# Kernel optimization log

Measured on AMD Instinct MI355X. Metric: run time of the kernel, lower is better.

Reference implementation:

```python
import jax, jax.numpy as jnp
import numpy as np

B, S, E, H, R = 512, 50, 128, 8, 32
D = E // H  # depth per head
USERS, ITEMS, ALLSEQ, NCLASS = 50000, 20000, 20000, 5


def setup_inputs() -> dict:
    key = jax.random.key(0)
    ks = jax.random.split(key, 20)
    n = lambda k, shp, s=0.05: jax.random.normal(k, shp, dtype=jnp.float32) * s
    return {
        "user": jax.random.randint(ks[0], (B,), 0, USERS),
        "item": jax.random.randint(ks[1], (B,), 0, ITEMS),
        "neighbor": jax.random.randint(ks[2], (B, S), 0, USERS),
        "seq": jax.random.randint(ks[3], (B, S), 0, ALLSEQ),
        "user_emb_table": n(ks[4], (USERS, E)),
        "item_emb_table": n(ks[5], (ITEMS, E)),
        "user_item_LCU": n(ks[6], (ALLSEQ, R, E), 0.01),
        "item_user_LCU": n(ks[7], (ALLSEQ, R, E), 0.01),
        "wq": n(ks[8], (E, E)), "bq": jnp.zeros((E,), jnp.float32),
        "wk": n(ks[9], (E, E)), "bk": jnp.zeros((E,), jnp.float32),
        "wv": n(ks[10], (E, E)), "bv": jnp.zeros((E,), jnp.float32),
        "wo": n(ks[11], (E, E)), "bo": jnp.zeros((E,), jnp.float32),
        "fc_w": n(ks[12], (R, NCLASS)), "fc_b": jnp.zeros((NCLASS,), jnp.float32),
    }


def _forward(user, item, neighbor, seq,
             user_emb_table, item_emb_table, user_item_LCU, item_user_LCU,
             wq, bq, wk, bk, wv, bv, wo, bo, fc_w, fc_b):
    user_emb = user_emb_table[user]            # [B,E]
    neighbor_emb = user_emb_table[neighbor]    # [B,S,E]
    item_emb = item_emb_table[item]            # [B,E]
    weight = (neighbor > 0).astype(jnp.float32)  # [B,S] padding mask (1=real)

    # ---- single-query multi-head attention (use_attention=True) ----
    q = (user_emb @ wq + bq).reshape(B, H, D)                       # [B,H,D]
    k = (neighbor_emb @ wk + bk).reshape(B, S, H, D).transpose(0, 2, 1, 3)  # [B,H,S,D]
    v = (neighbor_emb @ wv + bv).reshape(B, S, H, D).transpose(0, 2, 1, 3)  # [B,H,S,D]
    logits = jnp.einsum('bhd,bhsd->bhs', q, k) / jnp.sqrt(jnp.float32(D))
    logits = logits + (1.0 - weight)[:, None, :] * (-1e9)           # mask padding
    attn = jax.nn.softmax(logits, axis=-1)                          # [B,H,S]
    ctx = attn[..., None] * v                                       # [B,H,S,D]
    ctx = ctx.transpose(0, 2, 1, 3).reshape(B, S, E)                # [B,S,E]
    neighbor_emb = ctx @ wo + bo                                    # [B,S,E]

    # ---- region embedding ----
    K_ui = user_item_LCU[seq]   # [B,S,R,E]
    K_iu = item_user_LCU[seq]   # [B,S,R,E]
    neighbor_profile = jnp.einsum('bsre,bse->bsr', K_iu, neighbor_emb)  # [B,S,R]
    item_profile = jnp.einsum('bsre,be->bsr', K_ui, item_emb)          # [B,S,R]
    neighbor_rating = neighbor_profile * item_profile * weight[:, :, None]
    user_rating_vector = jnp.max(neighbor_rating, axis=1)              # [B,R]

    # ---- rating classifier ----
    return jax.nn.softmax(user_rating_vector @ fc_w + fc_b, axis=-1)   # [B,NCLASS]


def reference(user, item, neighbor, seq,
              user_emb_table, item_emb_table, user_item_LCU, item_user_LCU,
              wq, bq, wk, bk, wv, bv, wo, bo, fc_w, fc_b):
    return _forward(user, item, neighbor, seq,
                    user_emb_table, item_emb_table, user_item_LCU, item_user_LCU,
                    wq, bq, wk, bk, wv, bv, wo, bo, fc_w, fc_b)
```

## Files before the change

### kernel.cpp

```cpp
#include <hip/hip_runtime.h>
#include <math.h>

#define BB 512
#define SS 50
#define EE 128
#define HH 8
#define RR 32
#define NC 5
#define NSEQ 20000
#define NBS (BB*SS)
#define LDK 136

typedef __attribute__((ext_vector_type(8))) __bf16 bf16x8;
typedef __attribute__((ext_vector_type(4))) float f32x4;
typedef __attribute__((ext_vector_type(4))) unsigned short us4;

__device__ __forceinline__ unsigned short f2bf(float f) {
    unsigned int u = __float_as_uint(f);
    unsigned int r = (u + 0x7fffu + ((u >> 16) & 1u)) >> 16;
    return (unsigned short)r;
}
__device__ __forceinline__ float dot4(const float4& a, const float4& b) {
    return a.x*b.x + a.y*b.y + a.z*b.z + a.w*b.w;
}
__device__ __forceinline__ float dot4v(const f32x4& a, const float4& b) {
    return a[0]*b.x + a[1]*b.y + a[2]*b.z + a[3]*b.w;
}

__global__ __launch_bounds__(128) void conv_kernel(const float* __restrict__ wv,
                                                   const float* __restrict__ wo,
                                                   unsigned short* __restrict__ wvT,
                                                   unsigned short* __restrict__ woT) {
    const int n = blockIdx.x & 127;
    const float* src = (blockIdx.x >> 7) ? wo : wv;
    unsigned short* dst = (blockIdx.x >> 7) ? woT : wvT;
    const int k = threadIdx.x;
    dst[n*EE + k] = f2bf(src[k*EE + n]);
}

__global__ __launch_bounds__(256) void hist_kernel(const int* __restrict__ seq,
                                                   int* __restrict__ hist) {
    int i = blockIdx.x * 256 + threadIdx.x;
    if (i < NBS) atomicAdd(&hist[seq[i]], 1);
}

__global__ __launch_bounds__(1024) void scan_kernel(int* __restrict__ hist,
                                                    int* __restrict__ hstart) {
    const int t = threadIdx.x;
    const int CH = 20;
    const int base = t * CH;
    int loc[CH];
    int s = 0;
    #pragma unroll
    for (int i = 0; i < CH; ++i) {
        int idx = base + i;
        int v = (idx < NSEQ) ? hist[idx] : 0;
        loc[i] = s; s += v;
    }
    const int lane = t & 63, w = t >> 6;
    int incl = s;
    #pragma unroll
    for (int off = 1; off < 64; off <<= 1) {
        int n = __shfl_up(incl, off);
        if (lane >= off) incl += n;
    }
    __shared__ int wsum[16];
    if (lane == 63) wsum[w] = incl;
    __syncthreads();
    if (t == 0) {
        int acc = 0;
        #pragma unroll
        for (int k = 0; k < 16; ++k) { int v = wsum[k]; wsum[k] = acc; acc += v; }
    }
    __syncthreads();
    const int excl = incl - s + wsum[w];
    #pragma unroll
    for (int i = 0; i < CH; ++i) {
        int idx = base + i;
        if (idx < NSEQ) {
            int e = excl + loc[i];
            hist[idx] = e;
            hstart[idx] = e;
        }
    }
    if (t == 0) hstart[NSEQ] = NBS;
}

__global__ __launch_bounds__(256) void scatter_kernel(const int* __restrict__ seq,
                                                      int* __restrict__ hist,
                                                      int* __restrict__ perm) {
    int i = blockIdx.x * 256 + threadIdx.x;
    if (i < NBS) {
        int pos = atomicAdd(&hist[seq[i]], 1);
        perm[pos] = i;
    }
}

__global__ __launch_bounds__(256, 4) void attn_kernel(
    const int* __restrict__ user,
    const int* __restrict__ neighbor,
    const float* __restrict__ uet,
    const float* __restrict__ wq, const float* __restrict__ bq,
    const float* __restrict__ wk, const float* __restrict__ bk,
    const float* __restrict__ bv, const float* __restrict__ bo,
    const unsigned short* __restrict__ wvT, const unsigned short* __restrict__ woT,
    float* __restrict__ ws_ne2)
{
    __shared__ unsigned short kA[64*LDK];
    __shared__ unsigned short qkvT[16][EE];
    __shared__ float ue[EE];
    __shared__ float qs[EE];
    __shared__ float qkb[HH];
    __shared__ float attn_s[HH][64];
    __shared__ float maskadd[64];

    const int b = blockIdx.x;
    const int t = threadIdx.x;

    if (t < EE) ue[t] = uet[(size_t)user[b]*EE + t];
    if (t < 64) maskadd[t] = (t < SS && neighbor[b*SS + t] > 0) ? 0.f : -1e9f;
    for (int idx = t; idx < SS*32; idx += 256) {
        int s = idx >> 5, g = idx & 31;
        float4 v = ((const float4*)(uet + (size_t)neighbor[b*SS + s]*EE))[g];
        us4 o; o.x = f2bf(v.x); o.y = f2bf(v.y); o.z = f2bf(v.z); o.w = f2bf(v.w);
        *(us4*)&kA[s*LDK + g*4] = o;
    }
    for (int idx = t; idx < 14*LDK; idx += 256) kA[50*LDK + idx] = 0;
    for (int idx = t; idx < 8*EE; idx += 256) qkvT[8 + (idx >> 7)][idx & 127] = 0;
    __syncthreads();

    if (t < EE) {
        float acc = bq[t];
        #pragma unroll 4
        for (int e = 0; e < EE; ++e) acc = fmaf(ue[e], wq[e*EE + t], acc);
        qs[t] = acc;
    }
    __syncthreads();

    {
        const int e = t >> 1, h0 = (t & 1) * 4;
        const float* wrow = wk + e*EE;
        #pragma unroll
        for (int j = 0; j < 4; ++j) {
            int h = h0 + j;
            float acc = 0.f;
            #pragma unroll
            for (int d = 0; d < 16; ++d) acc = fmaf(qs[h*16 + d], wrow[h*16 + d], acc);
            qkvT[h][e] = f2bf(acc);
        }
    }
    if (t < HH) {
        float acc = 0.f;
        #pragma unroll
        for (int d = 0; d < 16; ++d) acc = fmaf(qs[t*16 + d], bk[t*16 + d], acc);
        qkb[t] = acc;
    }
    __syncthreads();

    const int w    = t >> 6;
    const int l    = t & 63;
    const int lrow = l & 15;
    const int kg   = l >> 4;

    bf16x8 a0 = *(const bf16x8*)&kA[(w*16 + lrow)*LDK +  0 + kg*8];
    bf16x8 a1 = *(const bf16x8*)&kA[(w*16 + lrow)*LDK + 32 + kg*8];
    bf16x8 a2 = *(const bf16x8*)&kA[(w*16 + lrow)*LDK + 64 + kg*8];
    bf16x8 a3 = *(const bf16x8*)&kA[(w*16 + lrow)*LDK + 96 + kg*8];

    {
        bf16x8 b0 = *(const bf16x8*)&qkvT[lrow][ 0 + kg*8];
        bf16x8 b1 = *(const bf16x8*)&qkvT[lrow][32 + kg*8];
        bf16x8 b2 = *(const bf16x8*)&qkvT[lrow][64 + kg*8];
        bf16x8 b3 = *(const bf16x8*)&qkvT[lrow][96 + kg*8];
        f32x4 c = {0.f, 0.f, 0.f, 0.f};
        c = __builtin_amdgcn_mfma_f32_16x16x32_bf16(a0, b0, c, 0, 0, 0);
        c = __builtin_amdgcn_mfma_f32_16x16x32_bf16(a1, b1, c, 0, 0, 0);
        c = __builtin_amdgcn_mfma_f32_16x16x32_bf16(a2, b2, c, 0, 0, 0);
        c = __builtin_amdgcn_mfma_f32_16x16x32_bf16(a3, b3, c, 0, 0, 0);
        const int h = lrow;
        if (h < HH) {
            #pragma unroll
            for (int rg = 0; rg < 4; ++rg) {
                const int row = w*16 + kg*4 + rg;
                attn_s[h][row] = (c[rg] + qkb[h]) * 0.25f + maskadd[row];
            }
        }
    }
    __syncthreads();

    if (t < 64) {
        int h = t >> 3, ll = t & 7;
        float mx = -3e38f;
        #pragma unroll
        for (int i = 0; i < 7; ++i) { int s = i*8 + ll; if (s < SS) mx = fmaxf(mx, attn_s[h][s]); }
        mx = fmaxf(mx, __shfl_xor(mx, 1));
        mx = fmaxf(mx, __shfl_xor(mx, 2));
        mx = fmaxf(mx, __shfl_xor(mx, 4));
        float ev[7]; float sm_ = 0.f;
        #pragma unroll
        for (int i = 0; i < 7; ++i) {
            int s = i*8 + ll; ev[i] = 0.f;
            if (s < SS) { ev[i] = expf(attn_s[h][s] - mx); sm_ += ev[i]; }
        }
        sm_ += __shfl_xor(sm_, 1);
        sm_ += __shfl_xor(sm_, 2);
        sm_ += __shfl_xor(sm_, 4);
        float inv = 1.f / sm_;
        #pragma unroll
        for (int i = 0; i < 7; ++i) { int s = i*8 + ll; if (s < SS) attn_s[h][s] = ev[i] * inv; }
    }
    __syncthreads();

    f32x4 acc[8];
    #pragma unroll
    for (int nt = 0; nt < 8; ++nt) {
        const unsigned short* bp = wvT + (nt*16 + lrow)*EE + kg*8;
        bf16x8 b0 = *(const bf16x8*)&bp[0];
        bf16x8 b1 = *(const bf16x8*)&bp[32];
        bf16x8 b2 = *(const bf16x8*)&bp[64];
        bf16x8 b3 = *(const bf16x8*)&bp[96];
        f32x4 c = {0.f, 0.f, 0.f, 0.f};
        c = __builtin_amdgcn_mfma_f32_16x16x32_bf16(a0, b0, c, 0, 0, 0);
        c = __builtin_amdgcn_mfma_f32_16x16x32_bf16(a1, b1, c, 0, 0, 0);
        c = __builtin_amdgcn_mfma_f32_16x16x32_bf16(a2, b2, c, 0, 0, 0);
        c = __builtin_amdgcn_mfma_f32_16x16x32_bf16(a3, b3, c, 0, 0, 0);
        acc[nt] = c;
    }
    #pragma unroll
    for (int nt = 0; nt < 8; ++nt) {
        const int col = nt*16 + lrow;
        const float bvc = bv[col];
        #pragma unroll
        for (int rg = 0; rg < 4; ++rg) {
            const int row = w*16 + kg*4 + rg;
            const float av = (row < SS) ? attn_s[nt][row] : 0.f;
            kA[row*LDK + col] = f2bf((acc[nt][rg] + bvc) * av);
        }
    }
    __syncthreads();

    bf16x8 c0 = *(const bf16x8*)&kA[(w*16 + lrow)*LDK +  0 + kg*8];
    bf16x8 c1 = *(const bf16x8*)&kA[(w*16 + lrow)*LDK + 32 + kg*8];
    bf16x8 c2 = *(const bf16x8*)&kA[(w*16 + lrow)*LDK + 64 + kg*8];
    bf16x8 c3 = *(const bf16x8*)&kA[(w*16 + lrow)*LDK + 96 + kg*8];

    #pragma unroll
    for (int nt = 0; nt < 8; ++nt) {
        const unsigned short* bp = woT + (nt*16 + lrow)*EE + kg*8;
        bf16x8 b0 = *(const bf16x8*)&bp[0];
        bf16x8 b1 = *(const bf16x8*)&bp[32];
        bf16x8 b2 = *(const bf16x8*)&bp[64];
        bf16x8 b3 = *(const bf16x8*)&bp[96];
        f32x4 c = {0.f, 0.f, 0.f, 0.f};
        c = __builtin_amdgcn_mfma_f32_16x16x32_bf16(c0, b0, c, 0, 0, 0);
        c = __builtin_amdgcn_mfma_f32_16x16x32_bf16(c1, b1, c, 0, 0, 0);
        c = __builtin_amdgcn_mfma_f32_16x16x32_bf16(c2, b2, c, 0, 0, 0);
        c = __builtin_amdgcn_mfma_f32_16x16x32_bf16(c3, b3, c, 0, 0, 0);
        const int col = nt*16 + lrow;
        const float boc = bo[col];
        #pragma unroll
        for (int rg = 0; rg < 4; ++rg) {
            const int row = w*16 + kg*4 + rg;
            if (row < SS)
                ws_ne2[((size_t)b*SS + row)*EE + col] = c[rg] + boc;
        }
    }
}

__global__ __launch_bounds__(256, 6) void region_kernel(
    const int* __restrict__ neighbor, const int* __restrict__ item,
    const float* __restrict__ ui_lcu, const float* __restrict__ iu_lcu,
    const float* __restrict__ iet, const float* __restrict__ ws_ne2,
    const int* __restrict__ hstart, const int* __restrict__ perm,
    float* __restrict__ ws_rating)
{
    const int j = blockIdx.x;
    const int start = hstart[j];
    const int end   = hstart[j + 1];
    if (start >= end) return;

    const int t = threadIdx.x;
    const int r = t >> 3, l = t & 7;

    const f32x4* kiu_g = (const f32x4*)(iu_lcu + ((size_t)j*RR + r)*EE);
    const f32x4* kui_g = (const f32x4*)(ui_lcu + ((size_t)j*RR + r)*EE);
    f32x4 kiu_r[4], kui_r[4];
    #pragma unroll
    for (int i = 0; i < 4; ++i) {
        kiu_r[i] = __builtin_nontemporal_load(&kiu_g[l + 8*i]);
        kui_r[i] = __builtin_nontemporal_load(&kui_g[l + 8*i]);
    }

    for (int o = start; o < end; ++o) {
        const int bs = perm[o];
        const int b  = bs / SS;
        const float4* n4 = (const float4*)(ws_ne2 + (size_t)bs*EE);
        const float4* i4 = (const float4*)(iet + (size_t)item[b]*EE);

        float np_ = 0.f, ip_ = 0.f;
        #pragma unroll
        for (int i = 0; i < 4; ++i) {
            int c = l + 8*i;
            np_ += dot4v(kiu_r[i], n4[c]);
            ip_ += dot4v(kui_r[i], i4[c]);
        }
        np_ += __shfl_xor(np_, 1); np_ += __shfl_xor(np_, 2); np_ += __shfl_xor(np_, 4);
        ip_ += __shfl_xor(ip_, 1); ip_ += __shfl_xor(ip_, 2); ip_ += __shfl_xor(ip_, 4);

        const float w = (neighbor[bs] > 0) ? 1.f : 0.f;
        if (l == 0) ws_rating[(size_t)bs*RR + r] = np_ * ip_ * w;
    }
}

__global__ __launch_bounds__(256) void head_kernel(
    const float* __restrict__ ws_rating,
    const float* __restrict__ fc_w, const float* __restrict__ fc_b,
    float* __restrict__ out)
{
    __shared__ float part[8][RR];
    __shared__ float urv[RR];
    __shared__ float lg[NC];
    const int b = blockIdx.x, t = threadIdx.x;
    const int r = t & 31, sub = t >> 5;

    float m = -3e38f;
    for (int s = sub; s < SS; s += 8)
        m = fmaxf(m, ws_rating[((size_t)b*SS + s)*RR + r]);
    part[sub][r] = m;
    __syncthreads();
    if (t < RR) {
        float mm = part[0][t];
        #pragma unroll
        for (int k = 1; k < 8; ++k) mm = fmaxf(mm, part[k][t]);
        urv[t] = mm;
    }
    __syncthreads();
    if (t < NC) {
        float acc = fc_b[t];
        #pragma unroll
        for (int rr = 0; rr < RR; ++rr) acc = fmaf(urv[rr], fc_w[rr*NC + t], acc);
        lg[t] = acc;
    }
    __syncthreads();
    if (t < NC) {
        float mx = lg[0];
        #pragma unroll
        for (int c = 1; c < NC; ++c) mx = fmaxf(mx, lg[c]);
        float sm = 0.f;
        #pragma unroll
        for (int c = 0; c < NC; ++c) sm += expf(lg[c] - mx);
        out[b*NC + t] = expf(lg[t] - mx) / sm;
    }
}

extern "C" void kernel_launch(void* const* d_in, const int* in_sizes, int n_in,
                              void* d_out, int out_size, void* d_ws, size_t ws_size,
                              hipStream_t stream) {
    const int*   user     = (const int*)d_in[0];
    const int*   item     = (const int*)d_in[1];
    const int*   neighbor = (const int*)d_in[2];
    const int*   seq      = (const int*)d_in[3];
    const float* uet      = (const float*)d_in[4];
    const float* iet      = (const float*)d_in[5];
    const float* ui_lcu   = (const float*)d_in[6];
    const float* iu_lcu   = (const float*)d_in[7];
    const float* wq = (const float*)d_in[8];   const float* bq = (const float*)d_in[9];
    const float* wk = (const float*)d_in[10];  const float* bk = (const float*)d_in[11];
    const float* wv = (const float*)d_in[12];  const float* bv = (const float*)d_in[13];
    const float* wo = (const float*)d_in[14];  const float* bo = (const float*)d_in[15];
    const float* fcw = (const float*)d_in[16]; const float* fcb = (const float*)d_in[17];

    float* ws = (float*)d_ws;
    float* ws_ne2    = ws;
    float* ws_rating = ws_ne2 + (size_t)BB*SS*EE;
    unsigned short* wvT = (unsigned short*)(ws_rating + (size_t)BB*SS*RR);
    unsigned short* woT = wvT + EE*EE;
    int*   hist      = (int*)(woT + EE*EE);
    int*   hstart    = hist + NSEQ;
    int*   perm      = hstart + NSEQ + 1;
    float* out = (float*)d_out;

    hipLaunchKernelGGL(conv_kernel, dim3(256), dim3(128), 0, stream, wv, wo, wvT, woT);
    hipMemsetAsync(hist, 0, NSEQ * sizeof(int), stream);
    hipLaunchKernelGGL(hist_kernel, dim3((NBS + 255)/256), dim3(256), 0, stream, seq, hist);
    hipLaunchKernelGGL(scan_kernel, dim3(1), dim3(1024), 0, stream, hist, hstart);
    hipLaunchKernelGGL(scatter_kernel, dim3((NBS + 255)/256), dim3(256), 0, stream, seq, hist, perm);

    hipLaunchKernelGGL(attn_kernel, dim3(BB), dim3(256), 0, stream,
                       user, neighbor, uet,
                       wq, bq, wk, bk, bv, bo, wvT, woT, ws_ne2);

    hipLaunchKernelGGL(region_kernel, dim3(NSEQ), dim3(256), 0, stream,
                       neighbor, item, ui_lcu, iu_lcu, iet, ws_ne2, hstart, perm, ws_rating);

    hipLaunchKernelGGL(head_kernel, dim3(BB), dim3(256), 0, stream,
                       ws_rating, fcw, fcb, out);
}
```

Before: 175.6 us.

## Split region kernel into per-table halves and fuse weight conversion with histogram

The region kernel now launches twice as many blocks, and each block handles only one LCU table (item-user or user-item). It writes neighbor and item profiles to separate buffers, and the head kernel multiplies them before the max-reduction. This halves registers per block and doubles parallelism to hide gather latency, at the cost of extra workspace traffic and a second pass over perm. The weight transpose/bf16 conversion and the seq histogram are also fused into a single launch to save one kernel launch.

```diff
diff --git a/kernel.cpp b/kernel.cpp
--- a/kernel.cpp
+++ b/kernel.cpp
@@ -20,28 +20,25 @@
     unsigned int r = (u + 0x7fffu + ((u >> 16) & 1u)) >> 16;
     return (unsigned short)r;
 }
-__device__ __forceinline__ float dot4(const float4& a, const float4& b) {
-    return a.x*b.x + a.y*b.y + a.z*b.z + a.w*b.w;
-}
 __device__ __forceinline__ float dot4v(const f32x4& a, const float4& b) {
     return a[0]*b.x + a[1]*b.y + a[2]*b.z + a[3]*b.w;
 }
 
-__global__ __launch_bounds__(128) void conv_kernel(const float* __restrict__ wv,
+__global__ __launch_bounds__(256) void prep_kernel(const float* __restrict__ wv,
                                                    const float* __restrict__ wo,
                                                    unsigned short* __restrict__ wvT,
-                                                   unsigned short* __restrict__ woT) {
-    const int n = blockIdx.x & 127;
-    const float* src = (blockIdx.x >> 7) ? wo : wv;
-    unsigned short* dst = (blockIdx.x >> 7) ? woT : wvT;
-    const int k = threadIdx.x;
-    dst[n*EE + k] = f2bf(src[k*EE + n]);
-}
-
-__global__ __launch_bounds__(256) void hist_kernel(const int* __restrict__ seq,
+                                                   unsigned short* __restrict__ woT,
+                                                   const int* __restrict__ seq,
                                                    int* __restrict__ hist) {
-    int i = blockIdx.x * 256 + threadIdx.x;
-    if (i < NBS) atomicAdd(&hist[seq[i]], 1);
+    const int bid = blockIdx.x, t = threadIdx.x;
+    if (bid < 128) {
+        const int n = bid;
+        if (t < 128) wvT[n*EE + t] = f2bf(wv[t*EE + n]);
+        else         woT[n*EE + (t - 128)] = f2bf(wo[(t - 128)*EE + n]);
+    } else {
+        const int i = (bid - 128) * 256 + t;
+        if (i < NBS) atomicAdd(&hist[seq[i]], 1);
+    }
 }
 
 __global__ __launch_bounds__(1024) void scan_kernel(int* __restrict__ hist,
@@ -267,14 +264,16 @@
     }
 }
 
-__global__ __launch_bounds__(256, 6) void region_kernel(
+__global__ __launch_bounds__(256) void region_kernel(
     const int* __restrict__ neighbor, const int* __restrict__ item,
     const float* __restrict__ ui_lcu, const float* __restrict__ iu_lcu,
     const float* __restrict__ iet, const float* __restrict__ ws_ne2,
     const int* __restrict__ hstart, const int* __restrict__ perm,
-    float* __restrict__ ws_rating)
+    float* __restrict__ ws_np, float* __restrict__ ws_ip)
 {
-    const int j = blockIdx.x;
+    const int bid = blockIdx.x;
+    const bool ip_half = (bid >= NSEQ);
+    const int j = ip_half ? (bid - NSEQ) : bid;
     const int start = hstart[j];
     const int end   = hstart[j + 1];
     if (start >= end) return;
@@ -282,38 +281,37 @@
     const int t = threadIdx.x;
     const int r = t >> 3, l = t & 7;
 
-    const f32x4* kiu_g = (const f32x4*)(iu_lcu + ((size_t)j*RR + r)*EE);
-    const f32x4* kui_g = (const f32x4*)(ui_lcu + ((size_t)j*RR + r)*EE);
-    f32x4 kiu_r[4], kui_r[4];
-    #pragma unroll
-    for (int i = 0; i < 4; ++i) {
-        kiu_r[i] = __builtin_nontemporal_load(&kiu_g[l + 8*i]);
-        kui_r[i] = __builtin_nontemporal_load(&kui_g[l + 8*i]);
-    }
-
-    for (int o = start; o < end; ++o) {
-        const int bs = perm[o];
-        const int b  = bs / SS;
-        const float4* n4 = (const float4*)(ws_ne2 + (size_t)bs*EE);
-        const float4* i4 = (const float4*)(iet + (size_t)item[b]*EE);
-
-        float np_ = 0.f, ip_ = 0.f;
-        #pragma unroll
-        for (int i = 0; i < 4; ++i) {
-            int c = l + 8*i;
-            np_ += dot4v(kiu_r[i], n4[c]);
-            ip_ += dot4v(kui_r[i], i4[c]);
-        }
-        np_ += __shfl_xor(np_, 1); np_ += __shfl_xor(np_, 2); np_ += __shfl_xor(np_, 4);
-        ip_ += __shfl_xor(ip_, 1); ip_ += __shfl_xor(ip_, 2); ip_ += __shfl_xor(ip_, 4);
-
-        const float w = (neighbor[bs] > 0) ? 1.f : 0.f;
-        if (l == 0) ws_rating[(size_t)bs*RR + r] = np_ * ip_ * w;
+    const float* tab = ip_half ? ui_lcu : iu_lcu;
+    const f32x4* kg = (const f32x4*)(tab + ((size_t)j*RR + r)*EE);
+    f32x4 k0 = kg[l], k1 = kg[l + 8], k2 = kg[l + 16], k3 = kg[l + 24];
+
+    if (ip_half) {
+        for (int o = start; o < end; ++o) {
+            const int bs = perm[o];
+            const int b  = (unsigned)bs / SS;
+            const float4* v4 = (const float4*)(iet + (size_t)item[b]*EE);
+            float acc = dot4v(k0, v4[l]) + dot4v(k1, v4[l + 8])
+                      + dot4v(k2, v4[l + 16]) + dot4v(k3, v4[l + 24]);
+            acc += __shfl_xor(acc, 1); acc += __shfl_xor(acc, 2); acc += __shfl_xor(acc, 4);
+            if (l == 0) ws_ip[(size_t)bs*RR + r] = acc;
+        }
+    } else {
+        for (int o = start; o < end; ++o) {
+            const int bs = perm[o];
+            const float4* v4 = (const float4*)(ws_ne2 + (size_t)bs*EE);
+            float acc = dot4v(k0, v4[l]) + dot4v(k1, v4[l + 8])
+                      + dot4v(k2, v4[l + 16]) + dot4v(k3, v4[l + 24]);
+            acc += __shfl_xor(acc, 1); acc += __shfl_xor(acc, 2); acc += __shfl_xor(acc, 4);
+            if (l == 0) {
+                const float w = (neighbor[bs] > 0) ? 1.f : 0.f;
+                ws_np[(size_t)bs*RR + r] = acc * w;
+            }
+        }
     }
 }
 
 __global__ __launch_bounds__(256) void head_kernel(
-    const float* __restrict__ ws_rating,
+    const float* __restrict__ ws_np, const float* __restrict__ ws_ip,
     const float* __restrict__ fc_w, const float* __restrict__ fc_b,
     float* __restrict__ out)
 {
@@ -324,8 +322,10 @@
     const int r = t & 31, sub = t >> 5;
 
     float m = -3e38f;
-    for (int s = sub; s < SS; s += 8)
-        m = fmaxf(m, ws_rating[((size_t)b*SS + s)*RR + r]);
+    for (int s = sub; s < SS; s += 8) {
+        const size_t idx = ((size_t)b*SS + s)*RR + r;
+        m = fmaxf(m, ws_np[idx] * ws_ip[idx]);
+    }
     part[sub][r] = m;
     __syncthreads();
     if (t < RR) {
@@ -371,18 +371,19 @@
     const float* fcw = (const float*)d_in[16]; const float* fcb = (const float*)d_in[17];
 
     float* ws = (float*)d_ws;
-    float* ws_ne2    = ws;
-    float* ws_rating = ws_ne2 + (size_t)BB*SS*EE;
-    unsigned short* wvT = (unsigned short*)(ws_rating + (size_t)BB*SS*RR);
+    float* ws_ne2 = ws;
+    float* ws_np  = ws_ne2 + (size_t)BB*SS*EE;
+    float* ws_ip  = ws_np  + (size_t)BB*SS*RR;
+    unsigned short* wvT = (unsigned short*)(ws_ip + (size_t)BB*SS*RR);
     unsigned short* woT = wvT + EE*EE;
-    int*   hist      = (int*)(woT + EE*EE);
-    int*   hstart    = hist + NSEQ;
-    int*   perm      = hstart + NSEQ + 1;
+    int*   hist   = (int*)(woT + EE*EE);
+    int*   hstart = hist + NSEQ;
+    int*   perm   = hstart + NSEQ + 1;
     float* out = (float*)d_out;
 
-    hipLaunchKernelGGL(conv_kernel, dim3(256), dim3(128), 0, stream, wv, wo, wvT, woT);
     hipMemsetAsync(hist, 0, NSEQ * sizeof(int), stream);
-    hipLaunchKernelGGL(hist_kernel, dim3((NBS + 255)/256), dim3(256), 0, stream, seq, hist);
+    hipLaunchKernelGGL(prep_kernel, dim3(128 + (NBS + 255)/256), dim3(256), 0, stream,
+                       wv, wo, wvT, woT, seq, hist);
     hipLaunchKernelGGL(scan_kernel, dim3(1), dim3(1024), 0, stream, hist, hstart);
     hipLaunchKernelGGL(scatter_kernel, dim3((NBS + 255)/256), dim3(256), 0, stream, seq, hist, perm);
 
@@ -390,9 +391,10 @@
                        user, neighbor, uet,
                        wq, bq, wk, bk, bv, bo, wvT, woT, ws_ne2);
 
-    hipLaunchKernelGGL(region_kernel, dim3(NSEQ), dim3(256), 0, stream,
-                       neighbor, item, ui_lcu, iu_lcu, iet, ws_ne2, hstart, perm, ws_rating);
+    hipLaunchKernelGGL(region_kernel, dim3(2*NSEQ), dim3(256), 0, stream,
+                       neighbor, item, ui_lcu, iu_lcu, iet, ws_ne2, hstart, perm,
+                       ws_np, ws_ip);
 
     hipLaunchKernelGGL(head_kernel, dim3(BB), dim3(256), 0, stream,
-                       ws_rating, fcw, fcb, out);
-}
+                       ws_np, ws_ip, fcw, fcb, out);
+}
```

Result: slower. 182.2 us (+3.7%).

## Widen attention blocks to 1024 threads and fuse weight conversion with histogram

Applied to the files above, without the earlier changes.

The attention kernel now uses 1024 threads per batch row. The four wave groups split the V and O projection column tiles, and the Q and K-fold dot products are spread over more threads with shuffle reductions. The weight transpose/bf16 conversion and the seq histogram are merged into one launch to cut launch overhead, and the division in the region kernel is made unsigned. The wider blocks give more parallelism per row, but the A fragments are reloaded redundantly per wave, and the larger block size may limit occupancy.

```diff
diff --git a/kernel.cpp b/kernel.cpp
--- a/kernel.cpp
+++ b/kernel.cpp
@@ -20,28 +20,25 @@
     unsigned int r = (u + 0x7fffu + ((u >> 16) & 1u)) >> 16;
     return (unsigned short)r;
 }
-__device__ __forceinline__ float dot4(const float4& a, const float4& b) {
-    return a.x*b.x + a.y*b.y + a.z*b.z + a.w*b.w;
-}
 __device__ __forceinline__ float dot4v(const f32x4& a, const float4& b) {
     return a[0]*b.x + a[1]*b.y + a[2]*b.z + a[3]*b.w;
 }
 
-__global__ __launch_bounds__(128) void conv_kernel(const float* __restrict__ wv,
+__global__ __launch_bounds__(256) void prep_kernel(const float* __restrict__ wv,
                                                    const float* __restrict__ wo,
                                                    unsigned short* __restrict__ wvT,
-                                                   unsigned short* __restrict__ woT) {
-    const int n = blockIdx.x & 127;
-    const float* src = (blockIdx.x >> 7) ? wo : wv;
-    unsigned short* dst = (blockIdx.x >> 7) ? woT : wvT;
-    const int k = threadIdx.x;
-    dst[n*EE + k] = f2bf(src[k*EE + n]);
-}
-
-__global__ __launch_bounds__(256) void hist_kernel(const int* __restrict__ seq,
+                                                   unsigned short* __restrict__ woT,
+                                                   const int* __restrict__ seq,
                                                    int* __restrict__ hist) {
-    int i = blockIdx.x * 256 + threadIdx.x;
-    if (i < NBS) atomicAdd(&hist[seq[i]], 1);
+    const int bid = blockIdx.x, t = threadIdx.x;
+    if (bid < 128) {
+        const int n = bid;
+        if (t < 128) wvT[n*EE + t] = f2bf(wv[t*EE + n]);
+        else         woT[n*EE + (t - 128)] = f2bf(wo[(t - 128)*EE + n]);
+    } else {
+        const int i = (bid - 128) * 256 + t;
+        if (i < NBS) atomicAdd(&hist[seq[i]], 1);
+    }
 }
 
 __global__ __launch_bounds__(1024) void scan_kernel(int* __restrict__ hist,
@@ -96,7 +93,7 @@
     }
 }
 
-__global__ __launch_bounds__(256, 4) void attn_kernel(
+__global__ __launch_bounds__(1024, 8) void attn_kernel(
     const int* __restrict__ user,
     const int* __restrict__ neighbor,
     const float* __restrict__ uet,
@@ -118,36 +115,42 @@
     const int t = threadIdx.x;
 
     if (t < EE) ue[t] = uet[(size_t)user[b]*EE + t];
-    if (t < 64) maskadd[t] = (t < SS && neighbor[b*SS + t] > 0) ? 0.f : -1e9f;
-    for (int idx = t; idx < SS*32; idx += 256) {
+    if (t >= 128 && t < 192) {
+        const int s = t - 128;
+        const bool real = (s < SS) && (neighbor[b*SS + s] > 0);
+        maskadd[s] = real ? 0.f : -1e9f;
+    }
+    for (int idx = t; idx < SS*32; idx += 1024) {
         int s = idx >> 5, g = idx & 31;
         float4 v = ((const float4*)(uet + (size_t)neighbor[b*SS + s]*EE))[g];
         us4 o; o.x = f2bf(v.x); o.y = f2bf(v.y); o.z = f2bf(v.z); o.w = f2bf(v.w);
         *(us4*)&kA[s*LDK + g*4] = o;
     }
-    for (int idx = t; idx < 14*LDK; idx += 256) kA[50*LDK + idx] = 0;
-    for (int idx = t; idx < 8*EE; idx += 256) qkvT[8 + (idx >> 7)][idx & 127] = 0;
-    __syncthreads();
-
-    if (t < EE) {
-        float acc = bq[t];
-        #pragma unroll 4
-        for (int e = 0; e < EE; ++e) acc = fmaf(ue[e], wq[e*EE + t], acc);
-        qs[t] = acc;
-    }
+    for (int idx = t; idx < 14*LDK; idx += 1024) kA[50*LDK + idx] = 0;
+    if (t < 8*EE) qkvT[8 + (t >> 7)][t & 127] = 0;
     __syncthreads();
 
     {
-        const int e = t >> 1, h0 = (t & 1) * 4;
-        const float* wrow = wk + e*EE;
-        #pragma unroll
-        for (int j = 0; j < 4; ++j) {
-            int h = h0 + j;
-            float acc = 0.f;
-            #pragma unroll
-            for (int d = 0; d < 16; ++d) acc = fmaf(qs[h*16 + d], wrow[h*16 + d], acc);
-            qkvT[h][e] = f2bf(acc);
-        }
+        const int col = t >> 3, sub = t & 7;
+        float acc = 0.f;
+        #pragma unroll
+        for (int d = 0; d < 16; ++d)
+            acc = fmaf(ue[sub*16 + d], wq[(sub*16 + d)*EE + col], acc);
+        acc += __shfl_xor(acc, 1);
+        acc += __shfl_xor(acc, 2);
+        acc += __shfl_xor(acc, 4);
+        if (sub == 0) qs[col] = acc + bq[col];
+    }
+    __syncthreads();
+
+    {
+        const int e = t >> 3, h = t & 7;
+        const float* wrow = wk + (size_t)e*EE + h*16;
+        float acc = 0.f;
+        #pragma unroll
+        for (int d = 0; d < 16; ++d)
+            acc = fmaf(qs[h*16 + d], wrow[d], acc);
+        qkvT[h][e] = f2bf(acc);
     }
     if (t < HH) {
         float acc = 0.f;
@@ -161,13 +164,15 @@
     const int l    = t & 63;
     const int lrow = l & 15;
     const int kg   = l >> 4;
-
-    bf16x8 a0 = *(const bf16x8*)&kA[(w*16 + lrow)*LDK +  0 + kg*8];
-    bf16x8 a1 = *(const bf16x8*)&kA[(w*16 + lrow)*LDK + 32 + kg*8];
-    bf16x8 a2 = *(const bf16x8*)&kA[(w*16 + lrow)*LDK + 64 + kg*8];
-    bf16x8 a3 = *(const bf16x8*)&kA[(w*16 + lrow)*LDK + 96 + kg*8];
-
-    {
+    const int rt   = w & 3;
+    const int np   = w >> 2;
+
+    bf16x8 a0 = *(const bf16x8*)&kA[(rt*16 + lrow)*LDK +  0 + kg*8];
+    bf16x8 a1 = *(const bf16x8*)&kA[(rt*16 + lrow)*LDK + 32 + kg*8];
+    bf16x8 a2 = *(const bf16x8*)&kA[(rt*16 + lrow)*LDK + 64 + kg*8];
+    bf16x8 a3 = *(const bf16x8*)&kA[(rt*16 + lrow)*LDK + 96 + kg*8];
+
+    if (np == 0) {
         bf16x8 b0 = *(const bf16x8*)&qkvT[lrow][ 0 + kg*8];
         bf16x8 b1 = *(const bf16x8*)&qkvT[lrow][32 + kg*8];
         bf16x8 b2 = *(const bf16x8*)&qkvT[lrow][64 + kg*8];
@@ -181,7 +186,7 @@
         if (h < HH) {
             #pragma unroll
             for (int rg = 0; rg < 4; ++rg) {
-                const int row = w*16 + kg*4 + rg;
+                const int row = rt*16 + kg*4 + rg;
                 attn_s[h][row] = (c[rg] + qkb[h]) * 0.25f + maskadd[row];
             }
         }
@@ -211,9 +216,9 @@
     }
     __syncthreads();
 
-    f32x4 acc[8];
-    #pragma unroll
-    for (int nt = 0; nt < 8; ++nt) {
+    #pragma unroll
+    for (int q = 0; q < 2; ++q) {
+        const int nt = np*2 + q;
         const unsigned short* bp = wvT + (nt*16 + lrow)*EE + kg*8;
         bf16x8 b0 = *(const bf16x8*)&bp[0];
         bf16x8 b1 = *(const bf16x8*)&bp[32];
@@ -224,28 +229,25 @@
         c = __builtin_amdgcn_mfma_f32_16x16x32_bf16(a1, b1, c, 0, 0, 0);
         c = __builtin_amdgcn_mfma_f32_16x16x32_bf16(a2, b2, c, 0, 0, 0);
         c = __builtin_amdgcn_mfma_f32_16x16x32_bf16(a3, b3, c, 0, 0, 0);
-        acc[nt] = c;
-    }
-    #pragma unroll
-    for (int nt = 0; nt < 8; ++nt) {
         const int col = nt*16 + lrow;
         const float bvc = bv[col];
         #pragma unroll
         for (int rg = 0; rg < 4; ++rg) {
-            const int row = w*16 + kg*4 + rg;
+            const int row = rt*16 + kg*4 + rg;
             const float av = (row < SS) ? attn_s[nt][row] : 0.f;
-            kA[row*LDK + col] = f2bf((acc[nt][rg] + bvc) * av);
-        }
-    }
-    __syncthreads();
-
-    bf16x8 c0 = *(const bf16x8*)&kA[(w*16 + lrow)*LDK +  0 + kg*8];
-    bf16x8 c1 = *(const bf16x8*)&kA[(w*16 + lrow)*LDK + 32 + kg*8];
-    bf16x8 c2 = *(const bf16x8*)&kA[(w*16 + lrow)*LDK + 64 + kg*8];
-    bf16x8 c3 = *(const bf16x8*)&kA[(w*16 + lrow)*LDK + 96 + kg*8];
-
-    #pragma unroll
-    for (int nt = 0; nt < 8; ++nt) {
+            kA[row*LDK + col] = f2bf((c[rg] + bvc) * av);
+        }
+    }
+    __syncthreads();
+
+    bf16x8 c0 = *(const bf16x8*)&kA[(rt*16 + lrow)*LDK +  0 + kg*8];
+    bf16x8 c1 = *(const bf16x8*)&kA[(rt*16 + lrow)*LDK + 32 + kg*8];
+    bf16x8 c2 = *(const bf16x8*)&kA[(rt*16 + lrow)*LDK + 64 + kg*8];
+    bf16x8 c3 = *(const bf16x8*)&kA[(rt*16 + lrow)*LDK + 96 + kg*8];
+
+    #pragma unroll
+    for (int q = 0; q < 2; ++q) {
+        const int nt = np*2 + q;
         const unsigned short* bp = woT + (nt*16 + lrow)*EE + kg*8;
         bf16x8 b0 = *(const bf16x8*)&bp[0];
         bf16x8 b1 = *(const bf16x8*)&bp[32];
@@ -260,7 +262,7 @@
         const float boc = bo[col];
         #pragma unroll
         for (int rg = 0; rg < 4; ++rg) {
-            const int row = w*16 + kg*4 + rg;
+            const int row = rt*16 + kg*4 + rg;
             if (row < SS)
                 ws_ne2[((size_t)b*SS + row)*EE + col] = c[rg] + boc;
         }
@@ -293,7 +295,7 @@
 
     for (int o = start; o < end; ++o) {
         const int bs = perm[o];
-        const int b  = bs / SS;
+        const int b  = (unsigned)bs / SS;
         const float4* n4 = (const float4*)(ws_ne2 + (size_t)bs*EE);
         const float4* i4 = (const float4*)(iet + (size_t)item[b]*EE);
 
@@ -380,13 +382,14 @@
     int*   perm      = hstart + NSEQ + 1;
     float* out = (float*)d_out;
 
-    hipLaunchKernelGGL(conv_kernel, dim3(256), dim3(128), 0, stream, wv, wo, wvT, woT);
     hipMemsetAsync(hist, 0, NSEQ * sizeof(int), stream);
-    hipLaunchKernelGGL(hist_kernel, dim3((NBS + 255)/256), dim3(256), 0, stream, seq, hist);
+    hipLaunchKernelGGL(prep_kernel, dim3(128 + (NBS + 255)/256), dim3(256), 0, stream,
+                       wv, wo, wvT, woT, seq, hist);
     hipLaunchKernelGGL(scan_kernel, dim3(1), dim3(1024), 0, stream, hist, hstart);
-    hipLaunchKernelGGL(scatter_kernel, dim3((NBS + 255)/256), dim3(256), 0, stream, seq, hist, perm);
-
-    hipLaunchKernelGGL(attn_kernel, dim3(BB), dim3(256), 0, stream,
+    hipLaunchKernelGGL(scatter_kernel, dim3((NBS + 255)/256), dim3(256), 0, stream,
+                       seq, hist, perm);
+
+    hipLaunchKernelGGL(attn_kernel, dim3(BB), dim3(1024), 0, stream,
                        user, neighbor, uet,
                        wq, bq, wk, bk, bv, bo, wvT, woT, ws_ne2);
 
```

New measurement: 167.0 us. 4.9% less time.
